# Kernel optimization log

Measured on AMD Instinct MI355X. Metric: run time of the kernel, lower is better.

Reference implementation:

```python
import jax, jax.numpy as jnp
import numpy as np

D_MODEL = 1024
N_HEADS = 16
D_K = D_MODEL // N_HEADS
SCALE = float(np.sqrt(D_K))


def setup_inputs() -> dict:
    key = jax.random.key(0)
    ks = jax.random.split(key, 12)
    B, S = 2, 2048
    std = 1.0 / np.sqrt(D_MODEL)
    inp = {
        "query": jax.random.normal(ks[0], (B, S, D_MODEL), jnp.float32),
        "key": jax.random.normal(ks[1], (B, S, D_MODEL), jnp.float32),
        "value": jax.random.normal(ks[2], (B, S, D_MODEL), jnp.float32),
        "mask": jnp.ones((B, S), jnp.int32),
        "Wq": jax.random.normal(ks[3], (D_MODEL, D_MODEL), jnp.float32) * std,
        "bq": jnp.zeros((D_MODEL,), jnp.float32),
        "Wk": jax.random.normal(ks[4], (D_MODEL, D_MODEL), jnp.float32) * std,
        "bk": jnp.zeros((D_MODEL,), jnp.float32),
        "Wv": jax.random.normal(ks[5], (D_MODEL, D_MODEL), jnp.float32) * std,
        "bv": jnp.zeros((D_MODEL,), jnp.float32),
        "Wo": jax.random.normal(ks[6], (D_MODEL, D_MODEL), jnp.float32) * std,
        "bo": jnp.zeros((D_MODEL,), jnp.float32),
    }
    return inp


def reference(query, key, value, mask, Wq, bq, Wk, bk, Wv, bv, Wo, bo):
    B, S, _ = query.shape
    # projections -> [B, H, S, d_k]
    def proj(x, W, b):
        return (x @ W.T + b).reshape(B, S, N_HEADS, D_K).transpose(0, 2, 1, 3)

    Q = proj(query, Wq, bq)
    K = proj(key, Wk, bk)
    V = proj(value, Wv, bv)
    # [B, H, Sq, Sk] scores
    scores = jnp.einsum("bhqd,bhkd->bhqk", Q, K) / SCALE
    m = mask[:, None, None, :]  # broadcast over heads and query positions
    scores = jnp.where(m == 0, jnp.float32(-1e9), scores)
    attn = jax.nn.softmax(scores, axis=-1)
    # dropout is identity in eval mode
    context = jnp.einsum("bhqk,bhkd->bhqd", attn, V)
    context = context.transpose(0, 2, 1, 3).reshape(B, S, D_MODEL)
    return context @ Wo.T + bo
```

## Files before the change

### kernel.cpp

```cpp
#include <hip/hip_runtime.h>
#include <stdint.h>

#define D_MODEL 1024
#define NH 16
#define DK 64
#define BATCH 2
#define SEQ 2048
#define MROWS (BATCH*SEQ)

typedef float f32x4 __attribute__((ext_vector_type(4)));
typedef __bf16 bf16x8 __attribute__((ext_vector_type(8)));

#define AS1 __attribute__((address_space(1)))
#define AS3 __attribute__((address_space(3)))

static __device__ __forceinline__ void gld_lds16(const void* g, void* l) {
    __builtin_amdgcn_global_load_lds((const AS1 unsigned int*)g,
                                     (AS3 unsigned int*)l, 16, 0, 0);
}

static __device__ __forceinline__ unsigned int f2bf(float f) {
    union { float f; unsigned int u; } v; v.f = f;
    return (v.u + 0x7fffu + ((v.u >> 16) & 1u)) >> 16;
}

struct PrepArgs {
    const float* src[7];
    unsigned short* dst[7];
    int n4[7];
};

__global__ __launch_bounds__(256) void prep_cvt(PrepArgs a) {
    const int z = blockIdx.y;
    const float4* s = (const float4*)a.src[z];
    ushort4* d = (ushort4*)a.dst[z];
    const int n = a.n4[z];
    for (int i = blockIdx.x * blockDim.x + threadIdx.x; i < n;
         i += gridDim.x * blockDim.x) {
        float4 v = s[i];
        ushort4 o;
        o.x = (unsigned short)f2bf(v.x);
        o.y = (unsigned short)f2bf(v.y);
        o.z = (unsigned short)f2bf(v.z);
        o.w = (unsigned short)f2bf(v.w);
        d[i] = o;
    }
}

struct GemmArgs {
    const unsigned short* A[3];
    const unsigned short* W[3];
    const float* bias[3];
    void* C[3];
    float scale[3];
};

template<bool OUT_F32>
__global__ __launch_bounds__(256) void gemm_bt(GemmArgs g) {
    __shared__ unsigned short As[128 * 64];
    __shared__ unsigned short Bs[128 * 64];
    const int z = blockIdx.z;
    const char* A = (const char*)g.A[z];
    const char* W = (const char*)g.W[z];
    const float* bias = g.bias[z];
    const float scale = g.scale[z];
    const int t = threadIdx.x;
    const int w = t >> 6, lane = t & 63;
    const int m0 = blockIdx.x * 128, n0 = blockIdx.y * 128;
    const int wm = (w >> 1) * 64, wn = (w & 1) * 64;

    const int srow = t >> 3;
    const int csw = ((t & 7) * 16) ^ ((srow & 7) << 4);
    const char* pA = A + (size_t)(m0 + srow) * 2048 + csw;
    const char* pW = W + (size_t)(n0 + srow) * 2048 + csw;

    f32x4 acc[4][4];
#pragma unroll
    for (int i = 0; i < 4; ++i)
#pragma unroll
        for (int j = 0; j < 4; ++j)
            acc[i][j] = (f32x4){0.f, 0.f, 0.f, 0.f};

    const int kg16 = (lane >> 4) * 16;
    const int swl = (lane & 7) << 4;

    for (int kt = 0; kt < 16; ++kt) {
        __syncthreads();
#pragma unroll
        for (int p = 0; p < 4; ++p) {
            gld_lds16(pA + (size_t)p * (32 * 2048), &As[w * 512 + p * 2048]);
            gld_lds16(pW + (size_t)p * (32 * 2048), &Bs[w * 512 + p * 2048]);
        }
        pA += 128; pW += 128;
        __syncthreads();
#pragma unroll
        for (int ks = 0; ks < 2; ++ks) {
            bf16x8 af[4], bfv[4];
#pragma unroll
            for (int i = 0; i < 4; ++i) {
                int ra = wm + i * 16 + (lane & 15);
                af[i] = *(const bf16x8*)((const char*)As + ra * 128 +
                                         ((ks * 64 + kg16) ^ swl));
                int rb = wn + i * 16 + (lane & 15);
                bfv[i] = *(const bf16x8*)((const char*)Bs + rb * 128 +
                                          ((ks * 64 + kg16) ^ swl));
            }
#pragma unroll
            for (int i = 0; i < 4; ++i)
#pragma unroll
                for (int j = 0; j < 4; ++j)
                    acc[i][j] = __builtin_amdgcn_mfma_f32_16x16x32_bf16(
                        af[i], bfv[j], acc[i][j], 0, 0, 0);
        }
    }

    float bj[4];
#pragma unroll
    for (int j = 0; j < 4; ++j) bj[j] = bias[n0 + wn + j * 16 + (lane & 15)];
#pragma unroll
    for (int i = 0; i < 4; ++i)
#pragma unroll
        for (int r = 0; r < 4; ++r) {
            int row = m0 + wm + i * 16 + (lane >> 4) * 4 + r;
#pragma unroll
            for (int j = 0; j < 4; ++j) {
                int col = n0 + wn + j * 16 + (lane & 15);
                float v = (acc[i][j][r] + bj[j]) * scale;
                if (OUT_F32)
                    ((float*)g.C[z])[(size_t)row * 1024 + col] = v;
                else
                    ((unsigned short*)g.C[z])[(size_t)row * 1024 + col] =
                        (unsigned short)f2bf(v);
            }
        }
}

__global__ __launch_bounds__(256) void attn_fwd(
    const unsigned short* __restrict__ Qb,
    const unsigned short* __restrict__ Kb,
    const unsigned short* __restrict__ Vb,
    const int* __restrict__ mask,
    unsigned short* __restrict__ Ctx) {
    __shared__ unsigned short Klds[64 * 64];
    __shared__ unsigned short Vt[64 * 64];
    __shared__ unsigned short Plds[4][32 * 64];

    const int qt = blockIdx.x, bh = blockIdx.y;
    const int b = bh >> 4, h = bh & 15;
    const int t = threadIdx.x, w = t >> 6, lane = t & 63;
    const size_t qrow0 = (size_t)b * SEQ + (size_t)qt * 128;
    const int wq0 = w * 32;
    const int kg16 = (lane >> 4) * 16;
    const int swl = (lane & 7) << 4;

    bf16x8 qf[2][2];
#pragma unroll
    for (int nf = 0; nf < 2; ++nf)
#pragma unroll
        for (int ks = 0; ks < 2; ++ks) {
            size_t row = qrow0 + wq0 + nf * 16 + (lane & 15);
            qf[nf][ks] = *(const bf16x8*)((const char*)Qb + row * 2048 +
                                          h * 128 + ks * 64 + kg16);
        }

    f32x4 cacc[2][4];
#pragma unroll
    for (int i = 0; i < 2; ++i)
#pragma unroll
        for (int j = 0; j < 4; ++j) cacc[i][j] = (f32x4){0.f, 0.f, 0.f, 0.f};
    float mstate[2] = {-3e38f, -3e38f};
    float lstate[2] = {0.f, 0.f};

    const char* Kbase = (const char*)Kb + ((size_t)b * SEQ) * 2048 + h * 128;
    const char* Vbase = (const char*)Vb + ((size_t)b * SEQ) * 2048 + h * 128;
    const int* mbase = mask + b * SEQ;

    const int srow = t >> 3;
    const int csw = ((t & 7) * 16) ^ ((srow & 7) << 4);
    const int k2 = t & 31, dblk = t >> 5;

    for (int kv = 0; kv < SEQ / 64; ++kv) {
        const int kv0 = kv * 64;
        __syncthreads();
#pragma unroll
        for (int p = 0; p < 2; ++p)
            gld_lds16(Kbase + (size_t)(kv0 + srow + p * 32) * 2048 + csw,
                      &Klds[w * 512 + p * 2048]);
        {
            const char* vr = Vbase + (size_t)(kv0 + 2 * k2) * 2048 + dblk * 16;
            uint4 va = *(const uint4*)vr;
            uint4 vb2 = *(const uint4*)(vr + 2048);
#pragma unroll
            for (int j = 0; j < 8; ++j) {
                unsigned int pa =
                    (((const unsigned int*)&va)[j >> 1] >> ((j & 1) * 16)) & 0xffffu;
                unsigned int pb =
                    (((const unsigned int*)&vb2)[j >> 1] >> ((j & 1) * 16)) & 0xffffu;
                int d = dblk * 8 + j;
                *(unsigned int*)((char*)Vt + d * 128 +
                                 ((4 * k2) ^ ((d & 7) << 4))) = pa | (pb << 16);
            }
        }
        __syncthreads();

        f32x4 sacc[4][2];
#pragma unroll
        for (int i = 0; i < 4; ++i)
#pragma unroll
            for (int j = 0; j < 2; ++j) sacc[i][j] = (f32x4){0.f, 0.f, 0.f, 0.f};
#pragma unroll
        for (int ks = 0; ks < 2; ++ks) {
            bf16x8 kf[4];
#pragma unroll
            for (int mf = 0; mf < 4; ++mf) {
                int r = mf * 16 + (lane & 15);
                kf[mf] = *(const bf16x8*)((const char*)Klds + r * 128 +
                                          ((ks * 64 + kg16) ^ swl));
            }
#pragma unroll
            for (int mf = 0; mf < 4; ++mf)
#pragma unroll
                for (int nf = 0; nf < 2; ++nf)
                    sacc[mf][nf] = __builtin_amdgcn_mfma_f32_16x16x32_bf16(
                        kf[mf], qf[nf][ks], sacc[mf][nf], 0, 0, 0);
        }

#pragma unroll
        for (int mf = 0; mf < 4; ++mf) {
            int4 mk = *(const int4*)(mbase + kv0 + mf * 16 + (lane >> 4) * 4);
#pragma unroll
            for (int r = 0; r < 4; ++r) {
                int mv = ((const int*)&mk)[r];
                if (mv == 0) {
#pragma unroll
                    for (int nf = 0; nf < 2; ++nf) sacc[mf][nf][r] = -1e9f;
                }
            }
        }

        float scalef[2];
#pragma unroll
        for (int nf = 0; nf < 2; ++nf) {
            float vm = -3e38f;
#pragma unroll
            for (int mf = 0; mf < 4; ++mf)
#pragma unroll
                for (int r = 0; r < 4; ++r) vm = fmaxf(vm, sacc[mf][nf][r]);
            vm = fmaxf(vm, __shfl_xor(vm, 16));
            vm = fmaxf(vm, __shfl_xor(vm, 32));
            float mnew = fmaxf(mstate[nf], vm);
            float sc = __expf(mstate[nf] - mnew);
            scalef[nf] = sc;
            mstate[nf] = mnew;
            float s = 0.f;
#pragma unroll
            for (int mf = 0; mf < 4; ++mf)
#pragma unroll
                for (int r = 0; r < 4; ++r) {
                    float p = __expf(sacc[mf][nf][r] - mnew);
                    sacc[mf][nf][r] = p;
                    s += p;
                }
            s += __shfl_xor(s, 16);
            s += __shfl_xor(s, 32);
            lstate[nf] = lstate[nf] * sc + s;
        }

#pragma unroll
        for (int mq = 0; mq < 2; ++mq)
#pragma unroll
            for (int r = 0; r < 4; ++r) {
                float sc = __shfl(scalef[mq], (lane >> 4) * 4 + r);
#pragma unroll
                for (int nd = 0; nd < 4; ++nd) cacc[mq][nd][r] *= sc;
            }

        unsigned short* Pw = &Plds[w][0];
#pragma unroll
        for (int nf = 0; nf < 2; ++nf)
#pragma unroll
            for (int mf = 0; mf < 4; ++mf) {
                int q = nf * 16 + (lane & 15);
                int kb = mf * 32 + (lane >> 4) * 8;
                unsigned int p0 = f2bf(sacc[mf][nf][0]) | (f2bf(sacc[mf][nf][1]) << 16);
                unsigned int p1 = f2bf(sacc[mf][nf][2]) | (f2bf(sacc[mf][nf][3]) << 16);
                int sw = (q & 7) << 4;
                *(unsigned int*)((char*)Pw + q * 128 + (kb ^ sw)) = p0;
                *(unsigned int*)((char*)Pw + q * 128 + ((kb + 4) ^ sw)) = p1;
            }

#pragma unroll
        for (int ks = 0; ks < 2; ++ks) {
            bf16x8 pa[2], vf[4];
#pragma unroll
            for (int mq = 0; mq < 2; ++mq) {
                int r = mq * 16 + (lane & 15);
                pa[mq] = *(const bf16x8*)((const char*)Pw + r * 128 +
                                          ((ks * 64 + kg16) ^ swl));
            }
#pragma unroll
            for (int nd = 0; nd < 4; ++nd) {
                int r = nd * 16 + (lane & 15);
                vf[nd] = *(const bf16x8*)((const char*)Vt + r * 128 +
                                          ((ks * 64 + kg16) ^ swl));
            }
#pragma unroll
            for (int mq = 0; mq < 2; ++mq)
#pragma unroll
                for (int nd = 0; nd < 4; ++nd)
                    cacc[mq][nd] = __builtin_amdgcn_mfma_f32_16x16x32_bf16(
                        pa[mq], vf[nd], cacc[mq][nd], 0, 0, 0);
        }
    }

#pragma unroll
    for (int mq = 0; mq < 2; ++mq)
#pragma unroll
        for (int r = 0; r < 4; ++r) {
            float li = __shfl(lstate[mq], (lane >> 4) * 4 + r);
            float inv = 1.f / li;
            size_t row = qrow0 + wq0 + mq * 16 + (lane >> 4) * 4 + r;
#pragma unroll
            for (int nd = 0; nd < 4; ++nd) {
                int col = h * 64 + nd * 16 + (lane & 15);
                Ctx[row * 1024 + col] = (unsigned short)f2bf(cacc[mq][nd][r] * inv);
            }
        }
}

extern "C" void kernel_launch(void* const* d_in, const int* in_sizes, int n_in,
                              void* d_out, int out_size, void* d_ws, size_t ws_size,
                              hipStream_t stream) {
    const float* q   = (const float*)d_in[0];
    const float* k   = (const float*)d_in[1];
    const float* v   = (const float*)d_in[2];
    const int* mask  = (const int*)d_in[3];
    const float* Wq  = (const float*)d_in[4];
    const float* bq  = (const float*)d_in[5];
    const float* Wk  = (const float*)d_in[6];
    const float* bk  = (const float*)d_in[7];
    const float* Wv  = (const float*)d_in[8];
    const float* bv  = (const float*)d_in[9];
    const float* Wo  = (const float*)d_in[10];
    const float* bo  = (const float*)d_in[11];

    unsigned short* ws = (unsigned short*)d_ws;
    const size_t NX = (size_t)MROWS * D_MODEL;
    const size_t NW = (size_t)D_MODEL * D_MODEL;
    unsigned short* Xq  = ws;
    unsigned short* Xk  = Xq + NX;
    unsigned short* Xv  = Xk + NX;
    unsigned short* Wqb = Xv + NX;
    unsigned short* Wkb = Wqb + NW;
    unsigned short* Wvb = Wkb + NW;
    unsigned short* Wob = Wvb + NW;
    unsigned short* Qb  = Wob + NW;
    unsigned short* Kb  = Qb + NX;
    unsigned short* Vb  = Kb + NX;
    unsigned short* Cx  = Vb + NX;

    PrepArgs pa;
    pa.src[0] = q;  pa.src[1] = k;  pa.src[2] = v;
    pa.src[3] = Wq; pa.src[4] = Wk; pa.src[5] = Wv; pa.src[6] = Wo;
    pa.dst[0] = Xq;  pa.dst[1] = Xk;  pa.dst[2] = Xv;
    pa.dst[3] = Wqb; pa.dst[4] = Wkb; pa.dst[5] = Wvb; pa.dst[6] = Wob;
    for (int i = 0; i < 3; ++i) pa.n4[i] = (int)(NX / 4);
    for (int i = 3; i < 7; ++i) pa.n4[i] = (int)(NW / 4);
    prep_cvt<<<dim3(256, 7), dim3(256), 0, stream>>>(pa);

    GemmArgs gq;
    gq.A[0] = Xq;  gq.A[1] = Xk;  gq.A[2] = Xv;
    gq.W[0] = Wqb; gq.W[1] = Wkb; gq.W[2] = Wvb;
    gq.bias[0] = bq; gq.bias[1] = bk; gq.bias[2] = bv;
    gq.C[0] = Qb; gq.C[1] = Kb; gq.C[2] = Vb;
    gq.scale[0] = 0.125f; gq.scale[1] = 1.f; gq.scale[2] = 1.f;
    gemm_bt<false><<<dim3(32, 8, 3), dim3(256), 0, stream>>>(gq);

    attn_fwd<<<dim3(16, 32), dim3(256), 0, stream>>>(Qb, Kb, Vb, mask, Cx);

    GemmArgs go;
    go.A[0] = Cx; go.W[0] = Wob; go.bias[0] = bo; go.C[0] = d_out;
    go.scale[0] = 1.f;
    go.A[1] = go.A[2] = nullptr; go.W[1] = go.W[2] = nullptr;
    go.bias[1] = go.bias[2] = nullptr; go.C[1] = go.C[2] = nullptr;
    go.scale[1] = go.scale[2] = 1.f;
    gemm_bt<true><<<dim3(32, 8, 1), dim3(256), 0, stream>>>(go);
}
```

Baseline: 278.0 us.

## Double-buffer attention K/V tiles with head-major layouts and pre-transposed V

The QKV projection now writes Q and K in a head-major [B,H,S,64] layout, and a new kernel writes V transposed per head. The attention kernel can then stage both K and V tiles with async global-to-LDS loads into double buffers, replacing the per-iteration in-register V transpose and its two barriers. It also remaps workgroup IDs for L2 locality, skips mask application when a tile is all ones, raises MFMA issue priority with s_setprio, and tree-reduces the softmax max and sum. The cost is an extra transpose kernel launch, a pass over V, and scattered stores in the GEMM epilogue.

```diff
diff --git a/kernel.cpp b/kernel.cpp
--- a/kernel.cpp
+++ b/kernel.cpp
@@ -53,6 +53,7 @@
     const float* bias[3];
     void* C[3];
     float scale[3];
+    int hm[3];
 };
 
 template<bool OUT_F32>
@@ -64,6 +65,7 @@
     const char* W = (const char*)g.W[z];
     const float* bias = g.bias[z];
     const float scale = g.scale[z];
+    const int hm = g.hm[z];
     const int t = threadIdx.x;
     const int w = t >> 6, lane = t & 63;
     const int m0 = blockIdx.x * 128, n0 = blockIdx.y * 128;
@@ -105,12 +107,14 @@
                 bfv[i] = *(const bf16x8*)((const char*)Bs + rb * 128 +
                                           ((ks * 64 + kg16) ^ swl));
             }
+            __builtin_amdgcn_s_setprio(1);
 #pragma unroll
             for (int i = 0; i < 4; ++i)
 #pragma unroll
                 for (int j = 0; j < 4; ++j)
                     acc[i][j] = __builtin_amdgcn_mfma_f32_16x16x32_bf16(
                         af[i], bfv[j], acc[i][j], 0, 0, 0);
+            __builtin_amdgcn_s_setprio(0);
         }
     }
 
@@ -126,41 +130,78 @@
             for (int j = 0; j < 4; ++j) {
                 int col = n0 + wn + j * 16 + (lane & 15);
                 float v = (acc[i][j][r] + bj[j]) * scale;
-                if (OUT_F32)
+                if (OUT_F32) {
                     ((float*)g.C[z])[(size_t)row * 1024 + col] = v;
-                else
+                } else if (hm) {
+                    int bb = row >> 11, ss = row & 2047;
+                    int hh = col >> 6, dd = col & 63;
+                    ((unsigned short*)g.C[z])
+                        [(((size_t)(bb * 16 + hh) * 2048) + ss) * 64 + dd] =
+                        (unsigned short)f2bf(v);
+                } else {
                     ((unsigned short*)g.C[z])[(size_t)row * 1024 + col] =
                         (unsigned short)f2bf(v);
-            }
-        }
+                }
+            }
+        }
+}
+
+__global__ __launch_bounds__(256) void tr_v(
+    const unsigned short* __restrict__ Vflat,
+    unsigned short* __restrict__ VtT) {
+    __shared__ unsigned short T[64 * 66];
+    const int bh = blockIdx.y, b = bh >> 4, h = bh & 15;
+    const int s0 = blockIdx.x * 64;
+    const int t = threadIdx.x, row = t >> 3, ch = t & 7;
+#pragma unroll
+    for (int p = 0; p < 2; ++p) {
+        int r = p * 32 + row;
+        const unsigned int* src = (const unsigned int*)(
+            Vflat + ((size_t)(b * 2048 + s0 + r) * 1024) + h * 64 + ch * 8);
+        unsigned int v0 = src[0], v1 = src[1], v2 = src[2], v3 = src[3];
+        unsigned int* dst = (unsigned int*)&T[r * 66 + ch * 8];
+        dst[0] = v0; dst[1] = v1; dst[2] = v2; dst[3] = v3;
+    }
+    __syncthreads();
+#pragma unroll
+    for (int p = 0; p < 2; ++p) {
+        int d = p * 32 + row;
+        union { unsigned short u16[8]; uint4 v; } o;
+#pragma unroll
+        for (int j = 0; j < 8; ++j) o.u16[j] = T[(ch * 8 + j) * 66 + d];
+        *(uint4*)(VtT + ((size_t)bh * 64 + d) * 2048 + s0 + ch * 8) = o.v;
+    }
 }
 
 __global__ __launch_bounds__(256) void attn_fwd(
-    const unsigned short* __restrict__ Qb,
-    const unsigned short* __restrict__ Kb,
-    const unsigned short* __restrict__ Vb,
+    const unsigned short* __restrict__ Qh,
+    const unsigned short* __restrict__ Kh,
+    const unsigned short* __restrict__ VtT,
     const int* __restrict__ mask,
     unsigned short* __restrict__ Ctx) {
-    __shared__ unsigned short Klds[64 * 64];
-    __shared__ unsigned short Vt[64 * 64];
-    __shared__ unsigned short Plds[4][32 * 64];
-
-    const int qt = blockIdx.x, bh = blockIdx.y;
+    __shared__ unsigned short KlA[4096], KlB[4096];
+    __shared__ unsigned short VlA[4096], VlB[4096];
+    __shared__ unsigned short Plds[4][2048];
+
+    const int wg = blockIdx.x + (int)gridDim.x * blockIdx.y;
+    const int swzid = (wg & 7) * 64 + (wg >> 3);
+    const int qt = swzid & 15, bh = swzid >> 4;
     const int b = bh >> 4, h = bh & 15;
+
     const int t = threadIdx.x, w = t >> 6, lane = t & 63;
-    const size_t qrow0 = (size_t)b * SEQ + (size_t)qt * 128;
     const int wq0 = w * 32;
     const int kg16 = (lane >> 4) * 16;
     const int swl = (lane & 7) << 4;
 
+    const char* Qbase = (const char*)Qh + (size_t)bh * 2048 * 128;
     bf16x8 qf[2][2];
 #pragma unroll
     for (int nf = 0; nf < 2; ++nf)
 #pragma unroll
         for (int ks = 0; ks < 2; ++ks) {
-            size_t row = qrow0 + wq0 + nf * 16 + (lane & 15);
-            qf[nf][ks] = *(const bf16x8*)((const char*)Qb + row * 2048 +
-                                          h * 128 + ks * 64 + kg16);
+            int row = qt * 128 + wq0 + nf * 16 + (lane & 15);
+            qf[nf][ks] = *(const bf16x8*)(Qbase + (size_t)row * 128 +
+                                          ks * 64 + kg16);
         }
 
     f32x4 cacc[2][4];
@@ -171,37 +212,35 @@
     float mstate[2] = {-3e38f, -3e38f};
     float lstate[2] = {0.f, 0.f};
 
-    const char* Kbase = (const char*)Kb + ((size_t)b * SEQ) * 2048 + h * 128;
-    const char* Vbase = (const char*)Vb + ((size_t)b * SEQ) * 2048 + h * 128;
+    const char* Kbyte = (const char*)Kh + (size_t)bh * 2048 * 128;
+    const char* Vbyte = (const char*)VtT + (size_t)bh * 64 * 4096;
     const int* mbase = mask + b * SEQ;
 
     const int srow = t >> 3;
     const int csw = ((t & 7) * 16) ^ ((srow & 7) << 4);
-    const int k2 = t & 31, dblk = t >> 5;
-
-    for (int kv = 0; kv < SEQ / 64; ++kv) {
-        const int kv0 = kv * 64;
-        __syncthreads();
-#pragma unroll
-        for (int p = 0; p < 2; ++p)
-            gld_lds16(Kbase + (size_t)(kv0 + srow + p * 32) * 2048 + csw,
-                      &Klds[w * 512 + p * 2048]);
-        {
-            const char* vr = Vbase + (size_t)(kv0 + 2 * k2) * 2048 + dblk * 16;
-            uint4 va = *(const uint4*)vr;
-            uint4 vb2 = *(const uint4*)(vr + 2048);
-#pragma unroll
-            for (int j = 0; j < 8; ++j) {
-                unsigned int pa =
-                    (((const unsigned int*)&va)[j >> 1] >> ((j & 1) * 16)) & 0xffffu;
-                unsigned int pb =
-                    (((const unsigned int*)&vb2)[j >> 1] >> ((j & 1) * 16)) & 0xffffu;
-                int d = dblk * 8 + j;
-                *(unsigned int*)((char*)Vt + d * 128 +
-                                 ((4 * k2) ^ ((d & 7) << 4))) = pa | (pb << 16);
-            }
-        }
-        __syncthreads();
+    const size_t srow128 = (size_t)srow * 128;
+    const size_t srow4096 = (size_t)srow * 4096;
+
+    auto stage = [&](unsigned short* Kd, unsigned short* Vd, int kv0) {
+        const char* ks = Kbyte + (size_t)kv0 * 128;
+        gld_lds16(ks + srow128 + csw,               Kd + w * 512);
+        gld_lds16(ks + srow128 + 32 * 128 + csw,    Kd + 2048 + w * 512);
+        const char* vs = Vbyte + (size_t)kv0 * 2;
+        gld_lds16(vs + srow4096 + csw,              Vd + w * 512);
+        gld_lds16(vs + srow4096 + 32 * 4096 + csw,  Vd + 2048 + w * 512);
+    };
+
+    unsigned short* Pw = &Plds[w][0];
+
+    auto compute = [&](const unsigned short* Kl, const unsigned short* Vl,
+                       int kv0) {
+        int4 mk[4]; int allone = 1;
+#pragma unroll
+        for (int mf = 0; mf < 4; ++mf) {
+            mk[mf] = *(const int4*)(mbase + kv0 + mf * 16 + (lane >> 4) * 4);
+            allone &= (mk[mf].x != 0) & (mk[mf].y != 0) &
+                      (mk[mf].z != 0) & (mk[mf].w != 0);
+        }
 
         f32x4 sacc[4][2];
 #pragma unroll
@@ -214,53 +253,62 @@
 #pragma unroll
             for (int mf = 0; mf < 4; ++mf) {
                 int r = mf * 16 + (lane & 15);
-                kf[mf] = *(const bf16x8*)((const char*)Klds + r * 128 +
+                kf[mf] = *(const bf16x8*)((const char*)Kl + r * 128 +
                                           ((ks * 64 + kg16) ^ swl));
             }
+            __builtin_amdgcn_s_setprio(1);
 #pragma unroll
             for (int mf = 0; mf < 4; ++mf)
 #pragma unroll
                 for (int nf = 0; nf < 2; ++nf)
                     sacc[mf][nf] = __builtin_amdgcn_mfma_f32_16x16x32_bf16(
                         kf[mf], qf[nf][ks], sacc[mf][nf], 0, 0, 0);
-        }
-
-#pragma unroll
-        for (int mf = 0; mf < 4; ++mf) {
-            int4 mk = *(const int4*)(mbase + kv0 + mf * 16 + (lane >> 4) * 4);
-#pragma unroll
-            for (int r = 0; r < 4; ++r) {
-                int mv = ((const int*)&mk)[r];
-                if (mv == 0) {
-#pragma unroll
-                    for (int nf = 0; nf < 2; ++nf) sacc[mf][nf][r] = -1e9f;
+            __builtin_amdgcn_s_setprio(0);
+        }
+
+        if (!__all(allone)) {
+#pragma unroll
+            for (int mf = 0; mf < 4; ++mf)
+#pragma unroll
+                for (int r = 0; r < 4; ++r) {
+                    int mv = (&mk[mf].x)[r];
+                    if (mv == 0) {
+                        sacc[mf][0][r] = -1e9f;
+                        sacc[mf][1][r] = -1e9f;
+                    }
                 }
-            }
         }
 
         float scalef[2];
 #pragma unroll
         for (int nf = 0; nf < 2; ++nf) {
-            float vm = -3e38f;
-#pragma unroll
-            for (int mf = 0; mf < 4; ++mf)
-#pragma unroll
-                for (int r = 0; r < 4; ++r) vm = fmaxf(vm, sacc[mf][nf][r]);
+            float a0 = fmaxf(fmaxf(sacc[0][nf][0], sacc[0][nf][1]),
+                             fmaxf(sacc[0][nf][2], sacc[0][nf][3]));
+            float a1 = fmaxf(fmaxf(sacc[1][nf][0], sacc[1][nf][1]),
+                             fmaxf(sacc[1][nf][2], sacc[1][nf][3]));
+            float a2 = fmaxf(fmaxf(sacc[2][nf][0], sacc[2][nf][1]),
+                             fmaxf(sacc[2][nf][2], sacc[2][nf][3]));
+            float a3 = fmaxf(fmaxf(sacc[3][nf][0], sacc[3][nf][1]),
+                             fmaxf(sacc[3][nf][2], sacc[3][nf][3]));
+            float vm = fmaxf(fmaxf(a0, a1), fmaxf(a2, a3));
             vm = fmaxf(vm, __shfl_xor(vm, 16));
             vm = fmaxf(vm, __shfl_xor(vm, 32));
             float mnew = fmaxf(mstate[nf], vm);
             float sc = __expf(mstate[nf] - mnew);
             scalef[nf] = sc;
             mstate[nf] = mnew;
-            float s = 0.f;
-#pragma unroll
-            for (int mf = 0; mf < 4; ++mf)
-#pragma unroll
-                for (int r = 0; r < 4; ++r) {
-                    float p = __expf(sacc[mf][nf][r] - mnew);
-                    sacc[mf][nf][r] = p;
-                    s += p;
-                }
+            float ps[4];
+#pragma unroll
+            for (int mf = 0; mf < 4; ++mf) {
+                float p0 = __expf(sacc[mf][nf][0] - mnew);
+                float p1 = __expf(sacc[mf][nf][1] - mnew);
+                float p2 = __expf(sacc[mf][nf][2] - mnew);
+                float p3 = __expf(sacc[mf][nf][3] - mnew);
+                sacc[mf][nf][0] = p0; sacc[mf][nf][1] = p1;
+                sacc[mf][nf][2] = p2; sacc[mf][nf][3] = p3;
+                ps[mf] = (p0 + p1) + (p2 + p3);
+            }
+            float s = (ps[0] + ps[1]) + (ps[2] + ps[3]);
             s += __shfl_xor(s, 16);
             s += __shfl_xor(s, 32);
             lstate[nf] = lstate[nf] * sc + s;
@@ -275,7 +323,6 @@
                 for (int nd = 0; nd < 4; ++nd) cacc[mq][nd][r] *= sc;
             }
 
-        unsigned short* Pw = &Plds[w][0];
 #pragma unroll
         for (int nf = 0; nf < 2; ++nf)
 #pragma unroll
@@ -301,16 +348,30 @@
 #pragma unroll
             for (int nd = 0; nd < 4; ++nd) {
                 int r = nd * 16 + (lane & 15);
-                vf[nd] = *(const bf16x8*)((const char*)Vt + r * 128 +
+                vf[nd] = *(const bf16x8*)((const char*)Vl + r * 128 +
                                           ((ks * 64 + kg16) ^ swl));
             }
+            __builtin_amdgcn_s_setprio(1);
 #pragma unroll
             for (int mq = 0; mq < 2; ++mq)
 #pragma unroll
                 for (int nd = 0; nd < 4; ++nd)
                     cacc[mq][nd] = __builtin_amdgcn_mfma_f32_16x16x32_bf16(
                         pa[mq], vf[nd], cacc[mq][nd], 0, 0, 0);
-        }
+            __builtin_amdgcn_s_setprio(0);
+        }
+    };
+
+    stage(KlA, VlA, 0);
+    __syncthreads();
+    for (int i = 0; i < 16; ++i) {
+        const int kv0 = i * 128;
+        if (kv0 + 64 < SEQ) stage(KlB, VlB, kv0 + 64);
+        compute(KlA, VlA, kv0);
+        __syncthreads();
+        if (kv0 + 128 < SEQ) stage(KlA, VlA, kv0 + 128);
+        compute(KlB, VlB, kv0 + 64);
+        __syncthreads();
     }
 
 #pragma unroll
@@ -319,7 +380,8 @@
         for (int r = 0; r < 4; ++r) {
             float li = __shfl(lstate[mq], (lane >> 4) * 4 + r);
             float inv = 1.f / li;
-            size_t row = qrow0 + wq0 + mq * 16 + (lane >> 4) * 4 + r;
+            size_t row = (size_t)b * SEQ + qt * 128 + wq0 + mq * 16 +
+                         (lane >> 4) * 4 + r;
 #pragma unroll
             for (int nd = 0; nd < 4; ++nd) {
                 int col = h * 64 + nd * 16 + (lane & 15);
@@ -354,10 +416,10 @@
     unsigned short* Wkb = Wqb + NW;
     unsigned short* Wvb = Wkb + NW;
     unsigned short* Wob = Wvb + NW;
-    unsigned short* Qb  = Wob + NW;
-    unsigned short* Kb  = Qb + NX;
-    unsigned short* Vb  = Kb + NX;
-    unsigned short* Cx  = Vb + NX;
+    unsigned short* Qhd = Wob + NW;
+    unsigned short* Khd = Qhd + NX;
+    unsigned short* Vfl = Khd + NX;
+    unsigned short* Cx  = Vfl + NX;
 
     PrepArgs pa;
     pa.src[0] = q;  pa.src[1] = k;  pa.src[2] = v;
@@ -372,17 +434,20 @@
     gq.A[0] = Xq;  gq.A[1] = Xk;  gq.A[2] = Xv;
     gq.W[0] = Wqb; gq.W[1] = Wkb; gq.W[2] = Wvb;
     gq.bias[0] = bq; gq.bias[1] = bk; gq.bias[2] = bv;
-    gq.C[0] = Qb; gq.C[1] = Kb; gq.C[2] = Vb;
+    gq.C[0] = Qhd; gq.C[1] = Khd; gq.C[2] = Vfl;
     gq.scale[0] = 0.125f; gq.scale[1] = 1.f; gq.scale[2] = 1.f;
+    gq.hm[0] = 1; gq.hm[1] = 1; gq.hm[2] = 0;
     gemm_bt<false><<<dim3(32, 8, 3), dim3(256), 0, stream>>>(gq);
 
-    attn_fwd<<<dim3(16, 32), dim3(256), 0, stream>>>(Qb, Kb, Vb, mask, Cx);
+    tr_v<<<dim3(32, 32), dim3(256), 0, stream>>>(Vfl, Xv);
+
+    attn_fwd<<<dim3(16, 32), dim3(256), 0, stream>>>(Qhd, Khd, Xv, mask, Cx);
 
     GemmArgs go;
     go.A[0] = Cx; go.W[0] = Wob; go.bias[0] = bo; go.C[0] = d_out;
-    go.scale[0] = 1.f;
+    go.scale[0] = 1.f; go.hm[0] = 0;
     go.A[1] = go.A[2] = nullptr; go.W[1] = go.W[2] = nullptr;
     go.bias[1] = go.bias[2] = nullptr; go.C[1] = go.C[2] = nullptr;
-    go.scale[1] = go.scale[2] = 1.f;
+    go.scale[1] = go.scale[2] = 1.f; go.hm[1] = go.hm[2] = 0;
     gemm_bt<true><<<dim3(32, 8, 1), dim3(256), 0, stream>>>(go);
 }
```

Result: faster. 263.3 us (-5.3%).
